# Performance work log

Measured on AMD Instinct MI355X. Metric: run time of the kernel, lower is better.

Reference implementation:

```python
import jax, jax.numpy as jnp
import numpy as np

D = 4                      # corr_disp / max_displacement
K = 2 * D + 1              # window side -> K*K = 81 displacement channels
C = 256                    # in_channels


def shifted_patches(x, d):
    """x: [B,C,H,W] -> [B,C,K*K,H,W]; patch k=(dy*K+dx) is x shifted by
    (dy-d, dx-d) with zero padding (matches Correlation/NaiveAssemble2 indexing)."""
    B, Ch, H, W = x.shape
    xp = jnp.pad(x, ((0, 0), (0, 0), (d, d), (d, d)))
    k = 2 * d + 1
    sl = [xp[:, :, dy:dy + H, dx:dx + W] for dy in range(k) for dx in range(k)]
    return jnp.stack(sl, axis=2)


def conv2d(x, w, b, pad):
    y = jax.lax.conv_general_dilated(
        x, w, window_strides=(1, 1), padding=[(pad, pad), (pad, pad)],
        dimension_numbers=('NCHW', 'OIHW', 'NCHW'))
    return y + b[None, :, None, None]


def setup_inputs() -> dict:
    key = jax.random.key(0)
    ks = jax.random.split(key, 12)
    B, H, W = 2, 64, 64
    std = 0.01
    return {
        'feat':     jax.random.normal(ks[0], (B, C, H, W), jnp.float32),
        'feat_ref': jax.random.normal(ks[1], (B, C, H, W), jnp.float32),
        # ConcatUpdate conv stack: 2C->256 (1x1), 256->16 (3x3), 16->3 (3x3), 3->2 (3x3)
        'w1': jax.random.normal(ks[2], (256, 2 * C, 1, 1), jnp.float32) * std,
        'b1': jnp.zeros((256,), jnp.float32),
        'w2': jax.random.normal(ks[3], (16, 256, 3, 3), jnp.float32) * std,
        'b2': jnp.zeros((16,), jnp.float32),
        'w3': jax.random.normal(ks[4], (3, 16, 3, 3), jnp.float32) * std,
        'b3': jnp.zeros((3,), jnp.float32),
        'w4': jax.random.normal(ks[5], (2, 3, 3, 3), jnp.float32) * std,
        'b4': jnp.array([1.0, 0.0], jnp.float32),  # init_weights: bias[0]=1, bias[1]=0
    }


def reference(feat, feat_ref, w1, b1, w2, b2, w3, b3, w4, b4):
    # Correlation (cost volume over (2D+1)^2 displacements, kernel_size=1)
    patches = shifted_patches(feat_ref, D)                    # [B,C,K2,H,W]
    aff = jnp.einsum('bchw,bckhw->bkhw', feat, patches)       # [B,K2,H,W]
    # sum-normalize over displacement channels (use_softmax_norm=False)
    aff = aff / (jnp.sum(aff, axis=1, keepdims=True) + 1e-7)
    # NaiveAssemble2: windowed weighted gather of feat_ref
    aligned = jnp.einsum('bkhw,bckhw->bchw', aff, patches)    # [B,C,H,W]
    # ConcatUpdate
    cat = jnp.concatenate([feat, aligned], axis=1)            # [B,2C,H,W]
    h = conv2d(cat, w1, b1, 0)
    h = conv2d(h, w2, b2, 1)
    h = conv2d(h, w3, b3, 1)
    logits = conv2d(h, w4, b4, 1)                             # [B,2,H,W]
    score = jax.nn.softmax(logits, axis=1)
    return score[:, 0:1] * feat + score[:, 1:2] * aligned
```

## Files before the change

### kernel.cpp

```cpp
#include <hip/hip_runtime.h>
#include <hip/hip_bf16.h>
#include <math.h>

#define BATCH 2
#define CCH   256
#define HH    64
#define WW    64
#define PIX   (HH*WW)
#define K2    81
#define BP_N  (BATCH*PIX)

__global__ void k_transpose(const float* __restrict__ in, float* __restrict__ out) {
    __shared__ float tile[32][33];
    int b  = blockIdx.z;
    int p0 = blockIdx.x * 32;
    int c0 = blockIdx.y * 32;
    int tx = threadIdx.x;
    int ty = threadIdx.y;
    const float* ib = in  + (size_t)b * CCH * PIX;
    float*       ob = out + (size_t)b * CCH * PIX;
    #pragma unroll
    for (int i = 0; i < 4; i++) {
        int c = c0 + ty + i * 8;
        int p = p0 + tx;
        tile[ty + i * 8][tx] = ib[(size_t)c * PIX + p];
    }
    __syncthreads();
    #pragma unroll
    for (int i = 0; i < 4; i++) {
        int p = p0 + ty + i * 8;
        int c = c0 + tx;
        ob[(size_t)p * CCH + c] = tile[tx][ty + i * 8];
    }
}

__global__ void k_corr_assemble(const float* __restrict__ featT,
                                const float* __restrict__ refT,
                                float* __restrict__ alignedT) {
    int blk = blockIdx.x;
    int bp  = ((blk & 7) << 10) | (blk >> 3);
    int b  = bp >> 12;
    int p  = bp & 4095;
    int h  = p >> 6, w = p & 63;
    int tid = threadIdx.x;

    __shared__ float s_feat[256];
    __shared__ float s_aff[K2];
    __shared__ float s_affn[K2];
    __shared__ int   s_pix[K2];
    __shared__ float s_den;

    s_feat[tid] = featT[((size_t)bp << 8) + tid];
    if (tid < K2) {
        int dy = tid / 9, dx = tid - dy * 9;
        int y = h + dy - 4, x = w + dx - 4;
        s_pix[tid] = ((unsigned)y < 64u && (unsigned)x < 64u) ? ((y << 6) | x) : -1;
    }
    __syncthreads();

    const float* rb = refT + ((size_t)b << 20);

    int hw = tid >> 5;
    int j  = tid & 31;
    for (int it = 0; it < 11; it++) {
        int k = it * 8 + hw;
        float partial = 0.f;
        int pix = (k < K2) ? s_pix[k] : -1;
        if (pix >= 0) {
            const float* rp = rb + ((size_t)pix << 8);
            #pragma unroll
            for (int t = 0; t < 8; t++) {
                int c = 32 * t + j;
                partial = fmaf(s_feat[c], rp[c], partial);
            }
        }
        partial = __fadd_rn(partial, __shfl_xor(partial, 8));
        partial = __fadd_rn(partial, __shfl_xor(partial, 16));
        partial = __fadd_rn(partial, __shfl_xor(partial, 4));
        partial = __fadd_rn(partial, __shfl_xor(partial, 2));
        partial = __fadd_rn(partial, __shfl_xor(partial, 1));
        if (j == 0 && k < K2) s_aff[k] = partial;
    }
    __syncthreads();

    if (tid == 0) {
        float s = 0.f;
        for (int k = 0; k < K2; k++) s = __fadd_rn(s, s_aff[k]);
        s_den = __fadd_rn(s, 1e-7f);
    }
    __syncthreads();
    if (tid < K2) s_affn[tid] = __fdiv_rn(s_aff[tid], s_den);
    __syncthreads();

    int c = tid;
    float acc = 0.f;
    for (int k = 0; k < K2; k++) {
        int pix = s_pix[k];
        if (pix >= 0)
            acc = fmaf(s_affn[k], rb[((size_t)pix << 8) + c], acc);
    }
    alignedT[((size_t)bp << 8) + c] = acc;
}

__global__ void k_w1t(const float* __restrict__ w1, float* __restrict__ w1t) {
    __shared__ float tile[32][33];
    int c0 = blockIdx.x * 32;
    int o0 = blockIdx.y * 32;
    int tx = threadIdx.x;
    int ty = threadIdx.y;
    #pragma unroll
    for (int i = 0; i < 4; i++)
        tile[ty + i * 8][tx] = w1[(size_t)(o0 + ty + i * 8) * 512 + c0 + tx];
    __syncthreads();
    #pragma unroll
    for (int i = 0; i < 4; i++)
        w1t[(size_t)(c0 + ty + i * 8) * 256 + o0 + tx] = tile[tx][ty + i * 8];
}

__global__ void k_conv1(const float* __restrict__ featT,
                        const float* __restrict__ alignedT,
                        const float* __restrict__ w1t,
                        const float* __restrict__ b1,
                        float* __restrict__ h1) {
    __shared__ float s_a[32][68];
    __shared__ float s_b[32][68];
    int m0  = blockIdx.x * 64;
    int n0  = blockIdx.y * 64;
    int tid = threadIdx.x;
    int tx  = tid & 15;
    int ty  = tid >> 4;

    float acc[4][4] = {{0.f}};

    for (int kc = 0; kc < 16; kc++) {
        int c0 = kc * 32;
        const float* asrc;
        int coff;
        if (c0 < 256) { asrc = featT;    coff = c0; }
        else          { asrc = alignedT; coff = c0 - 256; }

        #pragma unroll
        for (int i = tid; i < 512; i += 256) {
            int cq = i & 7, px = i >> 3;
            float4 v = *(const float4*)(asrc + ((size_t)(m0 + px) << 8) + coff + (cq << 2));
            s_a[cq * 4 + 0][px] = v.x;
            s_a[cq * 4 + 1][px] = v.y;
            s_a[cq * 4 + 2][px] = v.z;
            s_a[cq * 4 + 3][px] = v.w;
        }
        #pragma unroll
        for (int i = tid; i < 512; i += 256) {
            int oq = i & 15, cc = i >> 4;
            float4 v = *(const float4*)(w1t + (size_t)(c0 + cc) * 256 + n0 + (oq << 2));
            *(float4*)&s_b[cc][oq << 2] = v;
        }
        __syncthreads();

        #pragma unroll 8
        for (int k = 0; k < 32; k++) {
            float4 av = *(const float4*)&s_a[k][ty << 2];
            float4 bv = *(const float4*)&s_b[k][tx << 2];
            acc[0][0] = fmaf(av.x, bv.x, acc[0][0]);
            acc[0][1] = fmaf(av.x, bv.y, acc[0][1]);
            acc[0][2] = fmaf(av.x, bv.z, acc[0][2]);
            acc[0][3] = fmaf(av.x, bv.w, acc[0][3]);
            acc[1][0] = fmaf(av.y, bv.x, acc[1][0]);
            acc[1][1] = fmaf(av.y, bv.y, acc[1][1]);
            acc[1][2] = fmaf(av.y, bv.z, acc[1][2]);
            acc[1][3] = fmaf(av.y, bv.w, acc[1][3]);
            acc[2][0] = fmaf(av.z, bv.x, acc[2][0]);
            acc[2][1] = fmaf(av.z, bv.y, acc[2][1]);
            acc[2][2] = fmaf(av.z, bv.z, acc[2][2]);
            acc[2][3] = fmaf(av.z, bv.w, acc[2][3]);
            acc[3][0] = fmaf(av.w, bv.x, acc[3][0]);
            acc[3][1] = fmaf(av.w, bv.y, acc[3][1]);
            acc[3][2] = fmaf(av.w, bv.z, acc[3][2]);
            acc[3][3] = fmaf(av.w, bv.w, acc[3][3]);
        }
        __syncthreads();
    }

    float4 bias = *(const float4*)(b1 + n0 + tx * 4);
    #pragma unroll
    for (int i = 0; i < 4; i++) {
        int px = m0 + ty * 4 + i;
        float4 v;
        v.x = acc[i][0] + bias.x;
        v.y = acc[i][1] + bias.y;
        v.z = acc[i][2] + bias.z;
        v.w = acc[i][3] + bias.w;
        *(float4*)(h1 + ((size_t)px << 8) + n0 + tx * 4) = v;
    }
}

__global__ void k_w2t(const float* __restrict__ w2, float* __restrict__ w2t) {
    int i = blockIdx.x * 256 + threadIdx.x;
    if (i >= 16 * 256 * 9) return;
    int o  = i / 2304;
    int r  = i % 2304;
    int c  = r / 9;
    int kk = r % 9;
    int cg = c >> 2, ci = c & 3;
    w2t[(((kk * 64 + cg) * 16 + o) << 2) + ci] = w2[i];
}

__global__ void k_conv2(const float* __restrict__ h1,
                        const float* __restrict__ w2t,
                        const float* __restrict__ b2,
                        float* __restrict__ h2) {
    __shared__ float s_in[3][18][68];
    int blk = blockIdx.x;
    int b   = blk >> 8;
    int r   = blk & 255;
    int y   = r >> 2;
    int w0  = (r & 3) * 16;
    int tid = threadIdx.x;
    int o   = tid & 15;
    int ps  = (tid >> 4) & 7;

    const float* hb = h1 + ((size_t)b << 20);

    float4 a0 = {0.f, 0.f, 0.f, 0.f};
    float4 a1 = {0.f, 0.f, 0.f, 0.f};

    for (int chunk = 0; chunk < 4; chunk++) {
        int c0 = chunk << 6;
        for (int i = tid; i < 3 * 18 * 16; i += 256) {
            int c4 = i & 15;
            int pi = (i >> 4) % 18;
            int ri = (i >> 4) / 18;
            int yy = y + ri - 1;
            int xx = w0 + pi - 1;
            float4 v = {0.f, 0.f, 0.f, 0.f};
            if ((unsigned)yy < 64u && (unsigned)xx < 64u)
                v = *(const float4*)(hb + ((size_t)((yy << 6) | xx) << 8) + c0 + (c4 << 2));
            *(float4*)&s_in[ri][pi][c4 << 2] = v;
        }
        __syncthreads();

        #pragma unroll
        for (int kk = 0; kk < 9; kk++) {
            int ky = kk / 3, kx = kk - ky * 3;
            const float* wp = w2t + (((size_t)(kk * 64 + (c0 >> 2)) * 16 + o) << 2);
            #pragma unroll 8
            for (int c4 = 0; c4 < 16; c4++) {
                float4 wv = *(const float4*)(wp + (c4 << 6));
                float4 i0 = *(const float4*)&s_in[ky][ps + kx][c4 << 2];
                float4 i1 = *(const float4*)&s_in[ky][ps + 8 + kx][c4 << 2];
                a0.x = fmaf(wv.x, i0.x, a0.x);
                a0.y = fmaf(wv.y, i0.y, a0.y);
                a0.z = fmaf(wv.z, i0.z, a0.z);
                a0.w = fmaf(wv.w, i0.w, a0.w);
                a1.x = fmaf(wv.x, i1.x, a1.x);
                a1.y = fmaf(wv.y, i1.y, a1.y);
                a1.z = fmaf(wv.z, i1.z, a1.z);
                a1.w = fmaf(wv.w, i1.w, a1.w);
            }
        }
        __syncthreads();
    }

    size_t bp0 = ((size_t)b << 12) + (y << 6) + w0;
    h2[(bp0 + ps) * 16 + o]     = ((a0.x + a0.y) + (a0.z + a0.w)) + b2[o];
    h2[(bp0 + ps + 8) * 16 + o] = ((a1.x + a1.y) + (a1.z + a1.w)) + b2[o];
}

__global__ void k_conv3(const float* __restrict__ h2,
                        const float* __restrict__ w3,
                        const float* __restrict__ b3,
                        float* __restrict__ h3) {
    int bp = blockIdx.x * 256 + threadIdx.x;
    if (bp >= BP_N) return;
    int b = bp >> 12;
    int p = bp & 4095;
    int h = p >> 6, w = p & 63;
    const float* hb = h2 + ((size_t)b << 16);

    float a0 = 0.f, a1 = 0.f, a2 = 0.f;
    #pragma unroll
    for (int kk = 0; kk < 9; kk++) {
        int ky = kk / 3, kx = kk - ky * 3;
        int y = h + ky - 1, x = w + kx - 1;
        if ((unsigned)y >= 64u || (unsigned)x >= 64u) continue;
        const float* ip = hb + (size_t)((y << 6) | x) * 16;
        #pragma unroll
        for (int c = 0; c < 16; c++) {
            float v = ip[c];
            int wi = c * 9 + kk;
            a0 = fmaf(w3[wi],       v, a0);
            a1 = fmaf(w3[144 + wi], v, a1);
            a2 = fmaf(w3[288 + wi], v, a2);
        }
    }
    h3[(size_t)bp * 3 + 0] = a0 + b3[0];
    h3[(size_t)bp * 3 + 1] = a1 + b3[1];
    h3[(size_t)bp * 3 + 2] = a2 + b3[2];
}

__global__ void k_score(const float* __restrict__ h3,
                        const float* __restrict__ w4,
                        const float* __restrict__ b4,
                        float2* __restrict__ score) {
    int bp = blockIdx.x * 256 + threadIdx.x;
    if (bp >= BP_N) return;
    int b = bp >> 12;
    int p = bp & 4095;
    int h = p >> 6, w = p & 63;
    const float* hb = h3 + (size_t)b * PIX * 3;

    float l0 = 0.f, l1 = 0.f;
    #pragma unroll
    for (int kk = 0; kk < 9; kk++) {
        int ky = kk / 3, kx = kk - ky * 3;
        int y = h + ky - 1, x = w + kx - 1;
        if ((unsigned)y >= 64u || (unsigned)x >= 64u) continue;
        const float* ip = hb + (size_t)((y << 6) | x) * 3;
        #pragma unroll
        for (int c = 0; c < 3; c++) {
            float v = ip[c];
            int wi = c * 9 + kk;
            l0 = fmaf(w4[wi],      v, l0);
            l1 = fmaf(w4[27 + wi], v, l1);
        }
    }
    l0 += b4[0];
    l1 += b4[1];

    float m  = fmaxf(l0, l1);
    float e0 = expf(l0 - m);
    float e1 = expf(l1 - m);
    float s  = e0 + e1;
    score[bp] = make_float2(e0 / s, e1 / s);
}

__global__ void k_blend(const float* __restrict__ feat,
                        const float* __restrict__ alignedT,
                        const float2* __restrict__ score,
                        float* __restrict__ out) {
    __shared__ float tile[32][33];
    int b  = blockIdx.z;
    int p0 = blockIdx.x * 32;
    int c0 = blockIdx.y * 32;
    int tx = threadIdx.x;
    int ty = threadIdx.y;

    const float* at = alignedT + ((size_t)b << 20);
    #pragma unroll
    for (int i = 0; i < 4; i++) {
        int p = p0 + ty + i * 8;
        tile[ty + i * 8][tx] = at[((size_t)p << 8) + c0 + tx];
    }
    __syncthreads();

    int p = p0 + tx;
    float2 s = score[(b << 12) + p];
    #pragma unroll
    for (int i = 0; i < 4; i++) {
        int c = c0 + ty + i * 8;
        size_t idx = (((size_t)(b * 256 + c)) << 12) + p;
        out[idx] = __fadd_rn(__fmul_rn(s.x, feat[idx]),
                             __fmul_rn(s.y, tile[tx][ty + i * 8]));
    }
}

extern "C" void kernel_launch(void* const* d_in, const int* in_sizes, int n_in,
                              void* d_out, int out_size, void* d_ws, size_t ws_size,
                              hipStream_t stream) {
    const float* feat     = (const float*)d_in[0];
    const float* feat_ref = (const float*)d_in[1];
    const float* w1 = (const float*)d_in[2];
    const float* b1 = (const float*)d_in[3];
    const float* w2 = (const float*)d_in[4];
    const float* b2 = (const float*)d_in[5];
    const float* w3 = (const float*)d_in[6];
    const float* b3 = (const float*)d_in[7];
    const float* w4 = (const float*)d_in[8];
    const float* b4 = (const float*)d_in[9];
    float* out = (float*)d_out;

    const size_t NCP = (size_t)BATCH * CCH * PIX;
    char* wsb = (char*)d_ws;
    float*  featT    = (float*)wsb;   wsb += NCP * 4;
    float*  refT     = (float*)wsb;   wsb += NCP * 4;
    float*  alignedT = (float*)wsb;   wsb += NCP * 4;
    float*  h1       = (float*)wsb;   wsb += NCP * 4;
    float*  h2       = (float*)wsb;   wsb += (size_t)BP_N * 16 * 4;
    float*  h3       = (float*)wsb;   wsb += (size_t)BP_N * 3 * 4;
    float2* sc       = (float2*)wsb;  wsb += (size_t)BP_N * 8;
    float*  w2t      = (float*)wsb;   wsb += (size_t)16 * 256 * 9 * 4;
    float*  w1t      = (float*)wsb;   wsb += (size_t)512 * 256 * 4;

    dim3 tb(32, 8, 1);
    dim3 tg(PIX / 32, CCH / 32, BATCH);
    k_transpose<<<tg, tb, 0, stream>>>(feat, featT);
    k_transpose<<<tg, tb, 0, stream>>>(feat_ref, refT);
    k_w2t<<<144, 256, 0, stream>>>(w2, w2t);
    k_w1t<<<dim3(16, 8, 1), tb, 0, stream>>>(w1, w1t);

    k_corr_assemble<<<BP_N, 256, 0, stream>>>(featT, refT, alignedT);
    k_conv1<<<dim3(BP_N / 64, 256 / 64, 1), 256, 0, stream>>>(featT, alignedT, w1t, b1, h1);
    k_conv2<<<BP_N / 16, 256, 0, stream>>>(h1, w2t, b2, h2);
    k_conv3<<<BP_N / 256, 256, 0, stream>>>(h2, w3, b3, h3);
    k_score<<<BP_N / 256, 256, 0, stream>>>(h3, w4, b4, sc);
    k_blend<<<tg, tb, 0, stream>>>(feat, alignedT, sc, out);
}
```

Before: 263.9 us.

## Process four horizontally adjacent pixels per block in correlation-assemble kernel

Each block now handles four adjacent output pixels in a row instead of one. It loads the shared 12-wide window of reference features once per row and reuses each loaded value across the overlapping 9-wide windows of all four pixels, in both the correlation and assembly phases. This cuts redundant global or L2 loads of refT by about 3x and reduces block count. The cost is higher register pressure (feature cache plus 36 partial sums per thread), which may lower occupancy, and many more shuffle reductions per block.

```diff
diff --git a/kernel.cpp b/kernel.cpp
--- a/kernel.cpp
+++ b/kernel.cpp
@@ -38,68 +38,124 @@
                                 const float* __restrict__ refT,
                                 float* __restrict__ alignedT) {
     int blk = blockIdx.x;
-    int bp  = ((blk & 7) << 10) | (blk >> 3);
-    int b  = bp >> 12;
-    int p  = bp & 4095;
-    int h  = p >> 6, w = p & 63;
+    int q   = ((blk & 7) << 8) | (blk >> 3);
+    int bp0 = q << 2;
+    int b   = bp0 >> 12;
+    int p0  = bp0 & 4095;
+    int h   = p0 >> 6, w0 = p0 & 63;
     int tid = threadIdx.x;
 
-    __shared__ float s_feat[256];
-    __shared__ float s_aff[K2];
-    __shared__ float s_affn[K2];
-    __shared__ int   s_pix[K2];
-    __shared__ float s_den;
-
-    s_feat[tid] = featT[((size_t)bp << 8) + tid];
-    if (tid < K2) {
-        int dy = tid / 9, dx = tid - dy * 9;
-        int y = h + dy - 4, x = w + dx - 4;
-        s_pix[tid] = ((unsigned)y < 64u && (unsigned)x < 64u) ? ((y << 6) | x) : -1;
+    __shared__ float s_feat[4][256];
+    __shared__ float s_aff[4][K2];
+    __shared__ float s_affn[4][K2];
+    __shared__ float s_den[4];
+
+    {
+        const float* fb = featT + ((size_t)bp0 << 8);
+        float4 v = *(const float4*)(fb + tid * 4);
+        int px = tid >> 6;
+        int cc = (tid * 4) & 255;
+        *(float4*)&s_feat[px][cc] = v;
     }
     __syncthreads();
 
     const float* rb = refT + ((size_t)b << 20);
-
     int hw = tid >> 5;
     int j  = tid & 31;
-    for (int it = 0; it < 11; it++) {
-        int k = it * 8 + hw;
-        float partial = 0.f;
-        int pix = (k < K2) ? s_pix[k] : -1;
-        if (pix >= 0) {
-            const float* rp = rb + ((size_t)pix << 8);
+
+    float f[4][8];
+    #pragma unroll
+    for (int p = 0; p < 4; p++)
+        #pragma unroll
+        for (int t = 0; t < 8; t++)
+            f[p][t] = s_feat[p][32 * t + j];
+
+    for (int it = 0; it < 2; it++) {
+        int dy = it * 8 + hw;
+        if (dy < 9) {
+            int yy = h + dy - 4;
+            float P[4][9];
             #pragma unroll
-            for (int t = 0; t < 8; t++) {
-                int c = 32 * t + j;
-                partial = fmaf(s_feat[c], rp[c], partial);
+            for (int p = 0; p < 4; p++)
+                #pragma unroll
+                for (int dx = 0; dx < 9; dx++) P[p][dx] = 0.f;
+
+            if ((unsigned)yy < 64u) {
+                const float* rowb = rb + (((size_t)yy << 6) << 8);
+                #pragma unroll
+                for (int t = 0; t < 8; t++) {
+                    #pragma unroll
+                    for (int pp = 0; pp < 12; pp++) {
+                        int xx = w0 + pp - 4;
+                        float rv = 0.f;
+                        if ((unsigned)xx < 64u)
+                            rv = rowb[((size_t)xx << 8) + 32 * t + j];
+                        #pragma unroll
+                        for (int p = 0; p < 4; p++) {
+                            int dx = pp - p;
+                            if (dx >= 0 && dx < 9)
+                                P[p][dx] = fmaf(f[p][t], rv, P[p][dx]);
+                        }
+                    }
+                }
             }
-        }
-        partial = __fadd_rn(partial, __shfl_xor(partial, 8));
-        partial = __fadd_rn(partial, __shfl_xor(partial, 16));
-        partial = __fadd_rn(partial, __shfl_xor(partial, 4));
-        partial = __fadd_rn(partial, __shfl_xor(partial, 2));
-        partial = __fadd_rn(partial, __shfl_xor(partial, 1));
-        if (j == 0 && k < K2) s_aff[k] = partial;
-    }
-    __syncthreads();
-
-    if (tid == 0) {
+            #pragma unroll
+            for (int p = 0; p < 4; p++) {
+                #pragma unroll
+                for (int dx = 0; dx < 9; dx++) {
+                    float v = P[p][dx];
+                    v = __fadd_rn(v, __shfl_xor(v, 8));
+                    v = __fadd_rn(v, __shfl_xor(v, 16));
+                    v = __fadd_rn(v, __shfl_xor(v, 4));
+                    v = __fadd_rn(v, __shfl_xor(v, 2));
+                    v = __fadd_rn(v, __shfl_xor(v, 1));
+                    if (j == 0) s_aff[p][dy * 9 + dx] = v;
+                }
+            }
+        }
+    }
+    __syncthreads();
+
+    if (tid < 4) {
         float s = 0.f;
-        for (int k = 0; k < K2; k++) s = __fadd_rn(s, s_aff[k]);
-        s_den = __fadd_rn(s, 1e-7f);
-    }
-    __syncthreads();
-    if (tid < K2) s_affn[tid] = __fdiv_rn(s_aff[tid], s_den);
+        for (int k = 0; k < K2; k++) s = __fadd_rn(s, s_aff[tid][k]);
+        s_den[tid] = __fadd_rn(s, 1e-7f);
+    }
+    __syncthreads();
+    for (int i = tid; i < 4 * K2; i += 256) {
+        int p = i / K2, k = i - p * K2;
+        s_affn[p][k] = __fdiv_rn(s_aff[p][k], s_den[p]);
+    }
     __syncthreads();
 
     int c = tid;
-    float acc = 0.f;
-    for (int k = 0; k < K2; k++) {
-        int pix = s_pix[k];
-        if (pix >= 0)
-            acc = fmaf(s_affn[k], rb[((size_t)pix << 8) + c], acc);
-    }
-    alignedT[((size_t)bp << 8) + c] = acc;
+    float acc[4] = {0.f, 0.f, 0.f, 0.f};
+    for (int dy = 0; dy < 9; dy++) {
+        int yy = h + dy - 4;
+        if ((unsigned)yy >= 64u) continue;
+        float A[4][9];
+        #pragma unroll
+        for (int p = 0; p < 4; p++)
+            #pragma unroll
+            for (int dx = 0; dx < 9; dx++) A[p][dx] = s_affn[p][dy * 9 + dx];
+        const float* rowb = rb + (((size_t)yy << 6) << 8) + c;
+        #pragma unroll
+        for (int pp = 0; pp < 12; pp++) {
+            int xx = w0 + pp - 4;
+            if ((unsigned)xx >= 64u) continue;
+            float rv = rowb[(size_t)xx << 8];
+            #pragma unroll
+            for (int p = 0; p < 4; p++) {
+                int dx = pp - p;
+                if (dx >= 0 && dx < 9)
+                    acc[p] = fmaf(A[p][dx], rv, acc[p]);
+            }
+        }
+    }
+    float* at = alignedT + ((size_t)bp0 << 8);
+    #pragma unroll
+    for (int p = 0; p < 4; p++)
+        at[((size_t)p << 8) + c] = acc[p];
 }
 
 __global__ void k_w1t(const float* __restrict__ w1, float* __restrict__ w1t) {
@@ -397,7 +453,7 @@
     k_w2t<<<144, 256, 0, stream>>>(w2, w2t);
     k_w1t<<<dim3(16, 8, 1), tb, 0, stream>>>(w1, w1t);
 
-    k_corr_assemble<<<BP_N, 256, 0, stream>>>(featT, refT, alignedT);
+    k_corr_assemble<<<BP_N / 4, 256, 0, stream>>>(featT, refT, alignedT);
     k_conv1<<<dim3(BP_N / 64, 256 / 64, 1), 256, 0, stream>>>(featT, alignedT, w1t, b1, h1);
     k_conv2<<<BP_N / 16, 256, 0, stream>>>(h1, w2t, b2, h2);
     k_conv3<<<BP_N / 256, 256, 0, stream>>>(h2, w3, b3, h3);
```

New measurement: 459.4 us. +74.1%, slower.
